# Kernel tuning notes

Measured on AMD Instinct MI355X. Metric: run time of the kernel, lower is better.

Reference implementation:

```python
import jax, jax.numpy as jnp
import numpy as np


def setup_inputs() -> dict:
    key = jax.random.key(0)
    ks = jax.random.split(key, 6)
    B, Din, Dout, K, L = 4096, 4096, 4096, 256, 4
    # scale params like kaiming-ish init to keep activations O(1)
    hin = jax.random.normal(ks[0], (B, Din), dtype=jnp.float32)
    S1s = jax.random.normal(ks[1], (L, Din, K), dtype=jnp.float32) / np.sqrt(Din)
    S2s = jax.random.normal(ks[2], (L, K, Dout), dtype=jnp.float32) / np.sqrt(K)
    U1s = jax.random.normal(ks[3], (L, K, Dout), dtype=jnp.float32) / np.sqrt(K)
    U2s = jax.random.normal(ks[4], (L, Din, K), dtype=jnp.float32) / np.sqrt(Din)
    bias = jax.random.normal(ks[5], (Dout,), dtype=jnp.float32)
    return {"hin": hin, "S1s": S1s, "S2s": S2s, "U1s": U1s, "U2s": U2s, "bias": bias}


def reference(hin, S1s, S2s, U1s, U2s, bias):
    # out = (sum_l (hin @ S1s_l @ U1s_l + hin @ U2s_l @ S2s_l) + bias) / (2 L)
    L = S1s.shape[0]
    a = jnp.einsum('bd,ldk->lbk', hin, S1s)      # [L, B, K]
    t1 = jnp.einsum('lbk,lko->bo', a, U1s)       # [B, Dout]
    b = jnp.einsum('bd,ldk->lbk', hin, U2s)      # [L, B, K]
    t2 = jnp.einsum('lbk,lko->bo', b, S2s)       # [B, Dout]
    return (t1 + t2 + bias) / (2.0 * L)
```

## Files before the change

kernel.cpp:

```cpp
#include <hip/hip_runtime.h>
#include <stdint.h>

typedef unsigned short u16;
typedef __bf16 bf16x8 __attribute__((ext_vector_type(8)));
typedef float f32x4 __attribute__((ext_vector_type(4)));

#define DIN 4096
#define DOUT 4096
#define BB 4096
#define KR 256
#define RK 2048

__device__ __forceinline__ u16 f2bf(float f) {
    union { float f; unsigned u; } v; v.f = f;
    unsigned r = v.u + 0x7FFFu + ((v.u >> 16) & 1u);
    return (u16)(r >> 16);
}

__device__ __forceinline__ void gl_lds16(const void* g, void* l) {
    __builtin_amdgcn_global_load_lds((const __attribute__((address_space(1))) void*)g,
                                     (__attribute__((address_space(3))) void*)l,
                                     16, 0, 0);
}

__global__ __launch_bounds__(256) void cvt_f32_bf16(const float* __restrict__ src,
                                                    u16* __restrict__ dst, int n8) {
    int i = blockIdx.x * blockDim.x + threadIdx.x;
    if (i >= n8) return;
    const float4* s = reinterpret_cast<const float4*>(src) + (size_t)i * 2;
    float4 a = s[0], b = s[1];
    uint4 o;
    o.x = f2bf(a.x) | ((unsigned)f2bf(a.y) << 16);
    o.y = f2bf(a.z) | ((unsigned)f2bf(a.w) << 16);
    o.z = f2bf(b.x) | ((unsigned)f2bf(b.y) << 16);
    o.w = f2bf(b.z) | ((unsigned)f2bf(b.w) << 16);
    reinterpret_cast<uint4*>(dst)[i] = o;
}

__global__ __launch_bounds__(256) void pack_w1t(const float* __restrict__ S1s,
                                                const float* __restrict__ U2s,
                                                u16* __restrict__ W1T) {
    __shared__ u16 lds[64][68];
    int b  = blockIdx.x;
    int bd = b & 63;
    int bk = (b >> 6) & 3;
    int lb = b >> 8;
    int l = lb >> 1, br = lb & 1;
    const float* src = (br ? U2s : S1s) + (size_t)l * DIN * KR;
    int t = threadIdx.x;
    int d0 = bd * 64, k0 = bk * 64;
    int r0 = l * 512 + br * 256 + k0;
    #pragma unroll
    for (int p = 0; p < 4; ++p) {
        int dl = p * 16 + (t >> 4);
        int kc = (t & 15) * 4;
        float4 v = *reinterpret_cast<const float4*>(src + (size_t)(d0 + dl) * KR + k0 + kc);
        ushort4 pk;
        pk.x = f2bf(v.x); pk.y = f2bf(v.y); pk.z = f2bf(v.z); pk.w = f2bf(v.w);
        *reinterpret_cast<ushort4*>(&lds[dl][kc]) = pk;
    }
    __syncthreads();
    #pragma unroll
    for (int p = 0; p < 2; ++p) {
        int kl = p * 32 + (t >> 3);
        int d8 = t & 7;
        u16 tmp[8];
        #pragma unroll
        for (int j = 0; j < 8; ++j) tmp[j] = lds[d8 * 8 + j][kl];
        uint4 o;
        o.x = tmp[0] | ((unsigned)tmp[1] << 16);
        o.y = tmp[2] | ((unsigned)tmp[3] << 16);
        o.z = tmp[4] | ((unsigned)tmp[5] << 16);
        o.w = tmp[6] | ((unsigned)tmp[7] << 16);
        *reinterpret_cast<uint4*>(W1T + (size_t)(r0 + kl) * DIN + d0 + d8 * 8) = o;
    }
}

__global__ __launch_bounds__(256) void pack_w2t(const float* __restrict__ U1s,
                                                const float* __restrict__ S2s,
                                                u16* __restrict__ W2T) {
    __shared__ u16 lds[64][68];
    int b  = blockIdx.x;
    int bo = b & 63;
    int bk = (b >> 6) & 3;
    int lb = b >> 8;
    int l = lb >> 1, br = lb & 1;
    const float* src = (br ? S2s : U1s) + (size_t)l * KR * DOUT;
    int t = threadIdx.x;
    int o0 = bo * 64, k0 = bk * 64;
    #pragma unroll
    for (int p = 0; p < 4; ++p) {
        int kl = p * 16 + (t >> 4);
        int ol = (t & 15) * 4;
        float4 v = *reinterpret_cast<const float4*>(src + (size_t)(k0 + kl) * DOUT + o0 + ol);
        ushort4 pk;
        pk.x = f2bf(v.x); pk.y = f2bf(v.y); pk.z = f2bf(v.z); pk.w = f2bf(v.w);
        *reinterpret_cast<ushort4*>(&lds[kl][ol]) = pk;
    }
    __syncthreads();
    #pragma unroll
    for (int p = 0; p < 2; ++p) {
        int ol = p * 32 + (t >> 3);
        int k8 = t & 7;
        u16 tmp[8];
        #pragma unroll
        for (int j = 0; j < 8; ++j) tmp[j] = lds[k8 * 8 + j][ol];
        uint4 o;
        o.x = tmp[0] | ((unsigned)tmp[1] << 16);
        o.y = tmp[2] | ((unsigned)tmp[3] << 16);
        o.z = tmp[4] | ((unsigned)tmp[5] << 16);
        o.w = tmp[6] | ((unsigned)tmp[7] << 16);
        *reinterpret_cast<uint4*>(W2T + (size_t)(o0 + ol) * RK + l * 512 + br * 256 + k0 + k8 * 8) = o;
    }
}

template <int BN, int MW, int EPI, int ND, int KD>
__global__ __launch_bounds__(512)
__attribute__((amdgpu_waves_per_eu(2, 2)))
void gemm9(const u16* __restrict__ A,
           const u16* __restrict__ Bt,
           void* __restrict__ Cv,
           const float* __restrict__ bias) {
    extern __shared__ char smem[];
    constexpr int BHB = (BN == 256) ? 16384 : 8192;
    constexpr int BROWS = BN / 2;
    constexpr int NW = 8 / MW;
    constexpr int MF = 128 / (16 * MW);
    constexpr int MROW = 128 / MW;
    char* ldsA = smem;
    char* ldsB = smem + 65536;

    const int tid = threadIdx.x;
    const int l = tid & 63;
    const int wv = tid >> 6;
    const int wr = wv / NW;
    const int wc = wv % NW;

    int bid = blockIdx.x;
    bid = (bid & 7) * 32 + (bid >> 3);
    const int mt = bid >> 4, nt = bid & 15;
    const int m0 = mt * 256, n0 = nt * BN;

    constexpr int NITER = KD >> 7;

    unsigned aoff[2], boff[2];
    {
        #pragma unroll
        for (int r = 0; r < 2; ++r) {
            int lin = (r * 512 + tid) * 16;
            int s = lin ^ (((lin >> 7) & 7) << 4);
            int e = s >> 1;
            unsigned o = (unsigned)(e >> 6) * (unsigned)KD + (unsigned)(e & 63);
            aoff[r] = (unsigned)m0 * (unsigned)KD + o;
            boff[r] = (unsigned)n0 * (unsigned)KD + o;
        }
    }

    auto issueA = [&](int h, int b, unsigned kb) {
        char* d = ldsA + (((b << 1) | h) * 16384) + tid * 16;
        gl_lds16(A + aoff[0] + (unsigned)h * 128u * KD + kb, d);
        gl_lds16(A + aoff[1] + (unsigned)h * 128u * KD + kb, d + 8192);
    };
    auto issueB = [&](int h, int b, unsigned kb) {
        char* d = ldsB + (((b << 1) | h) * BHB) + tid * 16;
        gl_lds16(Bt + boff[0] + (unsigned)h * (unsigned)BROWS * KD + kb, d);
        if constexpr (BN == 256)
            gl_lds16(Bt + boff[1] + (unsigned)h * (unsigned)BROWS * KD + kb, d + 8192);
    };

    const int cc0 = ((l >> 4) ^ (l & 7)) << 4;
    int rowAb[MF];
    #pragma unroll
    for (int m = 0; m < MF; ++m) rowAb[m] = ((wr * MROW + m * 16 + (l & 15)) * 128) | cc0;
    int rowBb[2];
    #pragma unroll
    for (int n = 0; n < 2; ++n) rowBb[n] = ((wc * 32 + n * 16 + (l & 15)) * 128) | cc0;

    f32x4 acc[2][2][MF][2] = {};
    bf16x8 afA[MF][2];
    bf16x8 bf0[2][2], bf1[2][2];

#define RDA(B_, H_) do { const char* Ah_ = ldsA + (((B_) << 1) | (H_)) * 16384;       \
    _Pragma("unroll") for (int m_ = 0; m_ < MF; ++m_) {                               \
        afA[m_][0] = *(const bf16x8*)(Ah_ + rowAb[m_]);                               \
        afA[m_][1] = *(const bf16x8*)(Ah_ + (rowAb[m_] ^ 64)); } } while (0)
#define RDB(DST, B_, H_) do { const char* Bh_ = ldsB + (((B_) << 1) | (H_)) * BHB;    \
    _Pragma("unroll") for (int n_ = 0; n_ < 2; ++n_) {                                \
        DST[n_][0] = *(const bf16x8*)(Bh_ + rowBb[n_]);                               \
        DST[n_][1] = *(const bf16x8*)(Bh_ + (rowBb[n_] ^ 64)); } } while (0)
#define MM(MH, NH, BREG) do {                                                         \
    __builtin_amdgcn_s_setprio(1);                                                    \
    _Pragma("unroll") for (int m_ = 0; m_ < MF; ++m_)                                 \
        _Pragma("unroll") for (int n_ = 0; n_ < 2; ++n_) {                            \
            acc[MH][NH][m_][n_] = __builtin_amdgcn_mfma_f32_16x16x32_bf16(            \
                afA[m_][0], BREG[n_][0], acc[MH][NH][m_][n_], 0, 0, 0);               \
            acc[MH][NH][m_][n_] = __builtin_amdgcn_mfma_f32_16x16x32_bf16(            \
                afA[m_][1], BREG[n_][1], acc[MH][NH][m_][n_], 0, 0, 0); }             \
    __builtin_amdgcn_s_setprio(0); } while (0)
#define VMW do { if constexpr (BN == 256)                                             \
                     asm volatile("s_waitcnt vmcnt(6)" ::: "memory");                 \
                 else asm volatile("s_waitcnt vmcnt(4)" ::: "memory"); } while (0)
#define PH(RDS, STG, HINT, MH, NH, BREG, GATE) do {                                   \
    RDS; STG;                                                                         \
    if ((HINT) && BN == 256) asm volatile("s_waitcnt lgkmcnt(8)" ::: "memory");       \
    __builtin_amdgcn_s_barrier();                                                     \
    asm volatile("s_waitcnt lgkmcnt(0)" ::: "memory");                                \
    MM(MH, NH, BREG);                                                                 \
    if (GATE) VMW;                                                                    \
    __builtin_amdgcn_s_barrier();                                                     \
} while (0)

    issueA(0, 0, 0);  issueB(0, 0, 0);  issueB(1, 0, 0);  issueA(1, 0, 0);
    issueA(0, 1, 64); issueB(0, 1, 64); issueB(1, 1, 64);
    VMW;
    __builtin_amdgcn_s_barrier();

    for (int J = 0; J < NITER; ++J) {
        const unsigned kc = (unsigned)J << 7;
        PH({ RDA(0, 0); RDB(bf0, 0, 0); }, issueA(1, 1, kc + 64),  1, 0, 0, bf0, 0);
        PH({ RDB(bf1, 0, 1); },            issueA(0, 0, kc + 128), 0, 0, 1, bf1, 0);
        PH({ RDA(0, 1); },                 issueB(0, 0, kc + 128), 0, 1, 1, bf1, 0);
        PH({},                             issueB(1, 0, kc + 128), 0, 1, 0, bf0, 1);
        PH({ RDA(1, 0); RDB(bf0, 1, 0); }, issueA(1, 0, kc + 128), 1, 0, 0, bf0, 0);
        PH({ RDB(bf1, 1, 1); },            issueA(0, 1, kc + 192), 0, 0, 1, bf1, 0);
        PH({ RDA(1, 1); },                 issueB(0, 1, kc + 192), 0, 1, 1, bf1, 0);
        PH({},                             issueB(1, 1, kc + 192), 0, 1, 0, bf0, 1);
    }
#undef RDA
#undef RDB
#undef MM
#undef VMW
#undef PH

    const int colc = l & 15, rb = (l >> 4) * 4;
    #pragma unroll
    for (int mh = 0; mh < 2; ++mh)
    #pragma unroll
    for (int nh = 0; nh < 2; ++nh)
    #pragma unroll
    for (int m = 0; m < MF; ++m)
    #pragma unroll
    for (int n = 0; n < 2; ++n) {
        int c = n0 + nh * (BN / 2) + wc * 32 + n * 16 + colc;
        int r0r = m0 + mh * 128 + wr * MROW + m * 16 + rb;
        if (EPI == 0) {
            u16* Cb = (u16*)Cv;
            #pragma unroll
            for (int j = 0; j < 4; ++j)
                Cb[(size_t)(r0r + j) * ND + c] = f2bf(acc[mh][nh][m][n][j]);
        } else {
            float* Cf = (float*)Cv;
            float bv = bias[c];
            #pragma unroll
            for (int j = 0; j < 4; ++j)
                Cf[(size_t)(r0r + j) * ND + c] = (acc[mh][nh][m][n][j] + bv) * 0.125f;
        }
    }
}

extern "C" void kernel_launch(void* const* d_in, const int* in_sizes, int n_in,
                              void* d_out, int out_size, void* d_ws, size_t ws_size,
                              hipStream_t stream) {
    const float* hin  = (const float*)d_in[0];
    const float* S1s  = (const float*)d_in[1];
    const float* S2s  = (const float*)d_in[2];
    const float* U1s  = (const float*)d_in[3];
    const float* U2s  = (const float*)d_in[4];
    const float* bias = (const float*)d_in[5];
    float* out = (float*)d_out;

    const size_t SZ_HIN = (size_t)BB * DIN * 2 + 512;
    const size_t SZ_W   = (size_t)RK * DIN * 2 + 512;
    const size_t SZ_A   = (size_t)BB * RK * 2 + 512;
    if (ws_size < SZ_HIN + SZ_W + SZ_A) return;
    u16* hinbf = (u16*)d_ws;
    u16* Wx    = (u16*)((char*)d_ws + SZ_HIN);
    u16* abf   = (u16*)((char*)d_ws + SZ_HIN + SZ_W);

    (void)hipFuncSetAttribute(reinterpret_cast<const void*>(&gemm9<128, 4, 0, RK, DIN>),
                              hipFuncAttributeMaxDynamicSharedMemorySize, 98304);
    (void)hipFuncSetAttribute(reinterpret_cast<const void*>(&gemm9<256, 2, 1, DOUT, RK>),
                              hipFuncAttributeMaxDynamicSharedMemorySize, 131072);

    pack_w1t<<<64 * 4 * 8, 256, 0, stream>>>(S1s, U2s, Wx);
    cvt_f32_bf16<<<(BB * DIN / 8) / 256, 256, 0, stream>>>(hin, hinbf, BB * DIN / 8);
    gemm9<128, 4, 0, RK, DIN><<<256, 512, 98304, stream>>>(hinbf, Wx, abf, nullptr);
    pack_w2t<<<64 * 4 * 8, 256, 0, stream>>>(U1s, S2s, Wx);
    gemm9<256, 2, 1, DOUT, RK><<<256, 512, 131072, stream>>>(abf, Wx, out, bias);
}
```

Measured before the change: 165.9 us.

## Restructure GEMM main loop to interleave loads, LDS reads and MFMA with fewer barriers

Replaces the eight-phase loop, which placed two barriers around every MFMA block, with a schedule of four phases per iteration. Each phase interleaves global-to-LDS issues, LDS fragment reads and two MFMA blocks, and ends with a single barrier. The first fragment reads are hoisted before the loop, and the vmcnt wait thresholds are lowered to match the new issue order. The aim is to cut barrier stalls and overlap LDS reads with matrix math, at the risk of LDS hazards if the tighter wait counts or buffer reuse order are wrong.

Measured after the change: 163.8 us. No clear change (-1.3%).

```diff
diff --git a/kernel.cpp b/kernel.cpp
--- a/kernel.cpp
+++ b/kernel.cpp
@@ -117,7 +117,7 @@
 template <int BN, int MW, int EPI, int ND, int KD>
 __global__ __launch_bounds__(512)
 __attribute__((amdgpu_waves_per_eu(2, 2)))
-void gemm9(const u16* __restrict__ A,
+void gemm8(const u16* __restrict__ A,
            const u16* __restrict__ Bt,
            void* __restrict__ Cv,
            const float* __restrict__ bias) {
@@ -198,39 +198,34 @@
                 afA[m_][1], BREG[n_][1], acc[MH][NH][m_][n_], 0, 0, 0); }             \
     __builtin_amdgcn_s_setprio(0); } while (0)
 #define VMW do { if constexpr (BN == 256)                                             \
-                     asm volatile("s_waitcnt vmcnt(6)" ::: "memory");                 \
-                 else asm volatile("s_waitcnt vmcnt(4)" ::: "memory"); } while (0)
-#define PH(RDS, STG, HINT, MH, NH, BREG, GATE) do {                                   \
-    RDS; STG;                                                                         \
-    if ((HINT) && BN == 256) asm volatile("s_waitcnt lgkmcnt(8)" ::: "memory");       \
-    __builtin_amdgcn_s_barrier();                                                     \
-    asm volatile("s_waitcnt lgkmcnt(0)" ::: "memory");                                \
-    MM(MH, NH, BREG);                                                                 \
-    if (GATE) VMW;                                                                    \
-    __builtin_amdgcn_s_barrier();                                                     \
-} while (0)
-
-    issueA(0, 0, 0);  issueB(0, 0, 0);  issueB(1, 0, 0);  issueA(1, 0, 0);
-    issueA(0, 1, 64); issueB(0, 1, 64); issueB(1, 1, 64);
+                     asm volatile("s_waitcnt vmcnt(4)" ::: "memory");                 \
+                 else asm volatile("s_waitcnt vmcnt(3)" ::: "memory"); } while (0)
+#define ENDP do { asm volatile("" ::: "memory");                                      \
+                  __builtin_amdgcn_s_barrier(); } while (0)
+
+    issueA(0, 0, 0);  issueB(0, 0, 0);
+    issueA(1, 0, 0);  issueB(1, 0, 0);
+    issueA(0, 1, 64); issueB(0, 1, 64);
     VMW;
     __builtin_amdgcn_s_barrier();
 
+    RDA(0, 0); RDB(bf0, 0, 0);
     for (int J = 0; J < NITER; ++J) {
-        const unsigned kc = (unsigned)J << 7;
-        PH({ RDA(0, 0); RDB(bf0, 0, 0); }, issueA(1, 1, kc + 64),  1, 0, 0, bf0, 0);
-        PH({ RDB(bf1, 0, 1); },            issueA(0, 0, kc + 128), 0, 0, 1, bf1, 0);
-        PH({ RDA(0, 1); },                 issueB(0, 0, kc + 128), 0, 1, 1, bf1, 0);
-        PH({},                             issueB(1, 0, kc + 128), 0, 1, 0, bf0, 1);
-        PH({ RDA(1, 0); RDB(bf0, 1, 0); }, issueA(1, 0, kc + 128), 1, 0, 0, bf0, 0);
-        PH({ RDB(bf1, 1, 1); },            issueA(0, 1, kc + 192), 0, 0, 1, bf1, 0);
-        PH({ RDA(1, 1); },                 issueB(0, 1, kc + 192), 0, 1, 1, bf1, 0);
-        PH({},                             issueB(1, 1, kc + 192), 0, 1, 0, bf0, 1);
+        const unsigned kc = ((unsigned)J << 7);
+        issueA(1, 1, kc + 64); RDB(bf1, 0, 1); MM(0, 0, bf0);
+        issueB(1, 1, kc + 64); MM(0, 1, bf1); RDA(0, 1); ENDP;
+        issueA(0, 0, kc + 128); MM(1, 1, bf1);
+        issueB(0, 0, kc + 128); MM(1, 0, bf0); VMW; RDA(1, 0); RDB(bf0, 1, 0); ENDP;
+        issueA(1, 0, kc + 128); RDB(bf1, 1, 1); MM(0, 0, bf0);
+        issueB(1, 0, kc + 128); MM(0, 1, bf1); RDA(1, 1); ENDP;
+        issueA(0, 1, kc + 192); MM(1, 1, bf1);
+        issueB(0, 1, kc + 192); MM(1, 0, bf0); VMW; RDA(0, 0); RDB(bf0, 0, 0); ENDP;
     }
 #undef RDA
 #undef RDB
 #undef MM
 #undef VMW
-#undef PH
+#undef ENDP
 
     const int colc = l & 15, rb = (l >> 4) * 4;
     #pragma unroll
@@ -277,14 +272,14 @@
     u16* Wx    = (u16*)((char*)d_ws + SZ_HIN);
     u16* abf   = (u16*)((char*)d_ws + SZ_HIN + SZ_W);
 
-    (void)hipFuncSetAttribute(reinterpret_cast<const void*>(&gemm9<128, 4, 0, RK, DIN>),
+    (void)hipFuncSetAttribute(reinterpret_cast<const void*>(&gemm8<128, 4, 0, RK, DIN>),
                               hipFuncAttributeMaxDynamicSharedMemorySize, 98304);
-    (void)hipFuncSetAttribute(reinterpret_cast<const void*>(&gemm9<256, 2, 1, DOUT, RK>),
+    (void)hipFuncSetAttribute(reinterpret_cast<const void*>(&gemm8<256, 2, 1, DOUT, RK>),
                               hipFuncAttributeMaxDynamicSharedMemorySize, 131072);
 
     pack_w1t<<<64 * 4 * 8, 256, 0, stream>>>(S1s, U2s, Wx);
     cvt_f32_bf16<<<(BB * DIN / 8) / 256, 256, 0, stream>>>(hin, hinbf, BB * DIN / 8);
-    gemm9<128, 4, 0, RK, DIN><<<256, 512, 98304, stream>>>(hinbf, Wx, abf, nullptr);
+    gemm8<128, 4, 0, RK, DIN><<<256, 512, 98304, stream>>>(hinbf, Wx, abf, nullptr);
     pack_w2t<<<64 * 4 * 8, 256, 0, stream>>>(U1s, S2s, Wx);
-    gemm9<256, 2, 1, DOUT, RK><<<256, 512, 131072, stream>>>(abf, Wx, out, bias);
-}
+    gemm8<256, 2, 1, DOUT, RK><<<256, 512, 131072, stream>>>(abf, Wx, out, bias);
+}
```
